# Kernel optimization log

Hardware: AMD Instinct MI355X
Metric: run time of the kernel (lower is better)

Reference implementation:

```python
import jax, jax.numpy as jnp
import numpy as np

N = 50000   # nodes
E = 800000  # edges (sparse adjacency nnz)
FI = 256    # input feature dim
FO = 64     # output feature dim per head
H = 8       # attention heads


def setup_inputs() -> dict:
    key = jax.random.key(0)
    ks = jax.random.split(key, 6)
    x = jax.random.normal(ks[0], (N, FI), dtype=jnp.float32)
    W = jax.random.normal(ks[1], (H, FI, FO), dtype=jnp.float32) * 0.05
    a = jax.random.normal(ks[2], (H, FO), dtype=jnp.float32) * 0.05
    b = jax.random.normal(ks[3], (H, FO), dtype=jnp.float32) * 0.05
    rows = jax.random.randint(ks[4], (E,), 0, N, dtype=jnp.int32)
    cols = jax.random.randint(ks[5], (E,), 0, N, dtype=jnp.int32)
    return {"x": x, "W": W, "a": a, "b": b, "rows": rows, "cols": cols}


def reference(x, W, a, b, rows, cols):
    # SparseGAT forward: per head linear -> edge scores -> sparse row softmax
    # -> sparse aggregation -> bias; heads averaged then ReLU.
    n = x.shape[0]
    h = W.shape[0]
    NEG_SLOPE = 0.2  # tf.nn.leaky_relu default alpha
    acc = None
    for i in range(h):  # small fixed loop over heads
        t = x @ W[i]                                   # [N, FO]
        aw = t @ a[i]                                  # [N]
        e = jax.nn.leaky_relu(aw[rows] + aw[cols], NEG_SLOPE)   # [E]
        # sparse softmax per row (segment softmax, numerically stable)
        m = jax.ops.segment_max(e, rows, num_segments=n)        # [N]
        ex = jnp.exp(e - m[rows])                                # [E]
        den = jax.ops.segment_sum(ex, rows, num_segments=n)      # [N]
        coef = ex / den[rows]                                    # [E]
        # sparse matmul: sum_j coef_ij * t_j
        agg = jax.ops.segment_sum(coef[:, None] * t[cols], rows, num_segments=n)
        agg = agg + b[i]
        acc = agg if acc is None else acc + agg
    return jax.nn.relu(acc / h)
```

## Files before the change

kernel.cpp:

```cpp
#include <hip/hip_runtime.h>
#include <hip/hip_bf16.h>
#include <hip/hip_fp16.h>


#define FI 256
#define FO 64
#define NH 8
#define FC 512
#define BM 128
#define NBIN 64

typedef _Float16 f16x8 __attribute__((ext_vector_type(8)));
typedef float f32x16 __attribute__((ext_vector_type(16)));
typedef float f32x8 __attribute__((ext_vector_type(8)));

__global__ __launch_bounds__(256)
void p1_wconv(const float* __restrict__ W, _Float16* __restrict__ Wth) {
  int idx = blockIdx.x * 256 + threadIdx.x;
  if (idx >= NH * FO * FI) return;
  int k = idx & (FI - 1);
  int f = (idx >> 8) & (FO - 1);
  int h = idx >> 14;
  Wth[idx] = (_Float16)W[((size_t)h * FI + k) * FO + f];
}

__global__ __launch_bounds__(512)
void k1_v3(const float* __restrict__ x, const _Float16* __restrict__ Wth,
           const float* __restrict__ a, _Float16* __restrict__ Th,
           float* __restrict__ aw, int N) {
  __shared__ _Float16 Xs[BM][136];
  const int bm = blockIdx.x * BM;
  const int t = threadIdx.x;
  const int w = t >> 6;
  const int lane = t & 63;
  const int l31 = lane & 31;
  const int hi = lane >> 5;
  const int kh = hi * 8;
  const _Float16* Wh = Wth + (size_t)w * (FO * FI);

  f32x16 acc[4][2];
  #pragma unroll
  for (int mr = 0; mr < 4; ++mr)
    #pragma unroll
    for (int wc = 0; wc < 2; ++wc) acc[mr][wc] = (f32x16)0.0f;

  #pragma unroll
  for (int k0 = 0; k0 < 2; ++k0) {
    if (k0) __syncthreads();
    #pragma unroll
    for (int r = 0; r < 8; ++r) {
      int i = t + r * 512;
      int row = i >> 5;
      int q = i & 31;
      float4 v = make_float4(0.f, 0.f, 0.f, 0.f);
      if (bm + row < N)
        v = reinterpret_cast<const float4*>(&x[(size_t)(bm + row) * FI + k0 * 128])[q];
      _Float16 o[4] = {(_Float16)v.x, (_Float16)v.y, (_Float16)v.z, (_Float16)v.w};
      *reinterpret_cast<uint2*>(&Xs[row][q * 4]) = *reinterpret_cast<uint2*>(o);
    }
    __syncthreads();
    #pragma unroll
    for (int kk = 0; kk < 8; ++kk) {
      f16x8 xf[4], wf[2];
      #pragma unroll
      for (int mr = 0; mr < 4; ++mr)
        xf[mr] = *reinterpret_cast<const f16x8*>(&Xs[mr * 32 + l31][kk * 16 + kh]);
      #pragma unroll
      for (int wc = 0; wc < 2; ++wc)
        wf[wc] = *reinterpret_cast<const f16x8*>(
            &Wh[(size_t)(wc * 32 + l31) * FI + k0 * 128 + kk * 16 + kh]);
      #pragma unroll
      for (int mr = 0; mr < 4; ++mr)
        #pragma unroll
        for (int wc = 0; wc < 2; ++wc)
          acc[mr][wc] =
              __builtin_amdgcn_mfma_f32_32x32x16_f16(wf[wc], xf[mr], acc[mr][wc], 0, 0, 0);
    }
  }


  float s4[4] = {0.f, 0.f, 0.f, 0.f};
  #pragma unroll
  for (int wc = 0; wc < 2; ++wc)
    #pragma unroll
    for (int reg = 0; reg < 16; ++reg) {
      float av = a[w * FO + wc * 32 + (reg & 3) + 8 * (reg >> 2) + 4 * hi];
      #pragma unroll
      for (int mr = 0; mr < 4; ++mr)
        s4[mr] = fmaf(acc[mr][wc][reg], av, s4[mr]);
    }
  #pragma unroll
  for (int mr = 0; mr < 4; ++mr) {
    float s = s4[mr] + __shfl_xor(s4[mr], 32);
    int n = bm + mr * 32 + l31;
    if (hi == 0 && n < N) aw[(size_t)n * NH + w] = s;
  }

  #pragma unroll
  for (int mr = 0; mr < 4; ++mr) {
    int n = bm + mr * 32 + l31;
    if (n >= N) continue;
    _Float16* rowp = Th + (size_t)n * FC + w * FO;
    #pragma unroll
    for (int wc = 0; wc < 2; ++wc)
      #pragma unroll
      for (int g = 0; g < 4; ++g) {
        _Float16 o[4] = {(_Float16)acc[mr][wc][4 * g + 0],
                         (_Float16)acc[mr][wc][4 * g + 1],
                         (_Float16)acc[mr][wc][4 * g + 2],
                         (_Float16)acc[mr][wc][4 * g + 3]};
        *reinterpret_cast<uint2*>(&rowp[wc * 32 + 8 * g + 4 * hi]) =
            *reinterpret_cast<uint2*>(o);
      }
  }
}

__global__ __launch_bounds__(256)
void b1_hist(const int* __restrict__ rows, int* __restrict__ deg, int E) {
  int e = blockIdx.x * 256 + threadIdx.x;
  if (e < E) atomicAdd(&deg[rows[e]], 1);
}

__global__ __launch_bounds__(256)
void b2a_blocksum(const int* __restrict__ deg, int* __restrict__ blocksums, int N) {
  __shared__ int red[256];
  const int t = threadIdx.x;
  const int base = blockIdx.x * 1024 + t * 4;
  int s = 0;
  #pragma unroll
  for (int j = 0; j < 4; ++j) { int i = base + j; if (i < N) s += deg[i]; }
  red[t] = s;
  __syncthreads();
  for (int off = 128; off; off >>= 1) {
    if (t < off) red[t] += red[t + off];
    __syncthreads();
  }
  if (t == 0) blocksums[blockIdx.x] = red[0];
}

__global__ __launch_bounds__(64)
void b2b_scanblocks(int* __restrict__ blocksums, int nb,
                    int* __restrict__ row_start, int N, int E) {
  const int lane = threadIdx.x;
  int carry = 0;
  for (int base = 0; base < nb; base += 64) {
    int i = base + lane;
    int v = (i < nb) ? blocksums[i] : 0;
    int inc = v;
    #pragma unroll
    for (int off = 1; off < 64; off <<= 1) {
      int t = __shfl_up(inc, off);
      if (lane >= off) inc += t;
    }
    if (i < nb) blocksums[i] = inc - v + carry;
    carry += __shfl(inc, 63);
  }
  if (lane == 0) row_start[N] = E;
}

__global__ __launch_bounds__(256)
void b2c_rescan(const int* __restrict__ deg, const int* __restrict__ blocksums,
                int* __restrict__ row_start, int* __restrict__ cursor,
                int* __restrict__ blockhist, int N, int nbp) {
  __shared__ int ts[256];
  __shared__ int hist[NBIN];
  const int t = threadIdx.x;
  const int base = blockIdx.x * 1024 + t * 4;
  if (t < NBIN) hist[t] = 0;
  int v[4]; int s = 0;
  #pragma unroll
  for (int j = 0; j < 4; ++j) { int i = base + j; v[j] = (i < N) ? deg[i] : 0; s += v[j]; }
  ts[t] = s;
  __syncthreads();
  for (int off = 1; off < 256; off <<= 1) {
    int add = (t >= off) ? ts[t - off] : 0;
    __syncthreads();
    ts[t] += add;
    __syncthreads();
  }
  int run = blocksums[blockIdx.x] + ts[t] - s;
  #pragma unroll
  for (int j = 0; j < 4; ++j) {
    int i = base + j;
    if (i < N) {
      row_start[i] = run; cursor[i] = run; run += v[j];
      atomicAdd(&hist[min(v[j], NBIN - 1)], 1);
    }
  }
  __syncthreads();
  if (t < NBIN) blockhist[t * nbp + blockIdx.x] = hist[t];
}

__global__ __launch_bounds__(256)
void b3_scatter(const int* __restrict__ rows, const int* __restrict__ cols,
                int* __restrict__ cursor, int* __restrict__ colperm, int E) {
  int e = blockIdx.x * 256 + threadIdx.x;
  if (e >= E) return;
  int pos = atomicAdd(&cursor[rows[e]], 1);
  colperm[pos] = cols[e];
}

__global__ __launch_bounds__(64)
void b5b_scan(int* __restrict__ blockhist, int nbp) {
  const int lane = threadIdx.x;
  int* rowp = blockhist + lane * nbp;
  int tot = 0;
  for (int c = 0; c < nbp / 4; ++c) {
    int4 v = reinterpret_cast<const int4*>(rowp)[c];
    tot += v.x + v.y + v.z + v.w;
  }
  int inc = tot;
  #pragma unroll
  for (int off = 1; off < 64; off <<= 1) {
    int t = __shfl_up(inc, off);
    if (lane >= off) inc += t;
  }
  int run = inc - tot;
  for (int c = 0; c < nbp / 4; ++c) {
    int4 v = reinterpret_cast<const int4*>(rowp)[c];
    int4 o;
    o.x = run; run += v.x;
    o.y = run; run += v.y;
    o.z = run; run += v.z;
    o.w = run; run += v.w;
    reinterpret_cast<int4*>(rowp)[c] = o;
  }
}

__global__ __launch_bounds__(256)
void b5c_scatter(const int* __restrict__ deg, const int* __restrict__ blockhist,
                 int* __restrict__ row_order, int N, int nbp) {
  __shared__ int cur[NBIN];
  const int t = threadIdx.x;
  if (t < NBIN) cur[t] = blockhist[t * nbp + blockIdx.x];
  __syncthreads();
  const int base = blockIdx.x * 1024 + t * 4;
  #pragma unroll
  for (int j = 0; j < 4; ++j) {
    int i = base + j;
    if (i < N) {
      int pos = atomicAdd(&cur[min(deg[i], NBIN - 1)], 1);
      row_order[pos] = i;
    }
  }
}

__global__ __launch_bounds__(256)
void k4_fused(const int* __restrict__ row_start, const int* __restrict__ colperm,
              const int* __restrict__ row_order,
              const float* __restrict__ aw, const _Float16* __restrict__ Th,
              const float* __restrict__ b, float* __restrict__ out, int N) {
  const int lane16 = threadIdx.x & 15;
  const int gbase  = threadIdx.x & 48;
  const int hi8    = lane16 >> 3;
  const int ri = blockIdx.x * 16 + (threadIdx.x >> 4);
  if (ri >= N) return;
  const int r = row_order[ri];

  const int s0 = row_start[r], s1 = row_start[r + 1];
  f32x8 awr = *reinterpret_cast<const f32x8*>(&aw[(size_t)r * NH]);

  float facc[4][8] = {};
  float dacc[NH] = {};

  for (int base = s0; base < s1; base += 16) {
    const int mm = min(16, s1 - base);
    const bool valid = lane16 < mm;
    int c_l = valid ? colperm[base + lane16] : 0;

    f32x8 awc = *reinterpret_cast<const f32x8*>(&aw[(size_t)c_l * NH]);
    float ex[NH];
    int pkv[4];
    #pragma unroll
    for (int h = 0; h < NH; ++h) {
      float s = awr[h] + awc[h];
      float lr = s > 0.f ? s : 0.2f * s;
      ex[h] = valid ? __expf(lr) : 0.f;
      dacc[h] += ex[h];
    }
    #pragma unroll
    for (int q = 0; q < 4; ++q) {
      __half2 h2 = __floats2half2_rn(ex[2 * q], ex[2 * q + 1]);
      pkv[q] = *reinterpret_cast<int*>(&h2);
    }

    for (int j = 0; j < mm; ++j) {
      int cj = __shfl(c_l, gbase + j);
      const _Float16* tp = Th + (size_t)cj * FC + lane16 * 8;
      f16x8 tv0 = *reinterpret_cast<const f16x8*>(tp);
      f16x8 tv1 = *reinterpret_cast<const f16x8*>(tp + 128);
      f16x8 tv2 = *reinterpret_cast<const f16x8*>(tp + 256);
      f16x8 tv3 = *reinterpret_cast<const f16x8*>(tp + 384);
      float eq[4];
      #pragma unroll
      for (int q = 0; q < 4; ++q) {
        int p = __shfl(pkv[q], gbase + j);
        float2 f2 = __half22float2(*reinterpret_cast<__half2*>(&p));
        eq[q] = hi8 ? f2.y : f2.x;
      }
      #pragma unroll
      for (int e = 0; e < 8; ++e) {
        facc[0][e] = fmaf(eq[0], (float)tv0[e], facc[0][e]);
        facc[1][e] = fmaf(eq[1], (float)tv1[e], facc[1][e]);
        facc[2][e] = fmaf(eq[2], (float)tv2[e], facc[2][e]);
        facc[3][e] = fmaf(eq[3], (float)tv3[e], facc[3][e]);
      }
    }
  }

  #pragma unroll
  for (int h = 0; h < NH; ++h) {
    #pragma unroll
    for (int off = 1; off < 16; off <<= 1)
      dacc[h] += __shfl_xor(dacc[h], off);
  }
  float rden[NH];
  #pragma unroll
  for (int h = 0; h < NH; ++h) rden[h] = dacc[h] > 0.f ? 1.0f / dacc[h] : 0.f;

  float s[8] = {};
  #pragma unroll
  for (int q = 0; q < 4; ++q) {
    float rd = hi8 ? rden[2 * q + 1] : rden[2 * q];
    #pragma unroll
    for (int e = 0; e < 8; ++e) s[e] = fmaf(facc[q][e], rd, s[e]);
  }
  #pragma unroll
  for (int e = 0; e < 8; ++e) s[e] += __shfl_xor(s[e], 8);

  if (lane16 < 8) {
    #pragma unroll
    for (int e = 0; e < 8; ++e) {
      const int f = lane16 * 8 + e;
      float sb = 0.f;
      #pragma unroll
      for (int h = 0; h < NH; ++h) sb += b[h * FO + f];
      float v = (s[e] + sb) * 0.125f;
      out[(size_t)r * FO + f] = v > 0.f ? v : 0.f;
    }
  }
}

extern "C" void kernel_launch(void* const* d_in, const int* in_sizes, int n_in,
                              void* d_out, int out_size, void* d_ws, size_t ws_size,
                              hipStream_t stream) {
  const float* x    = (const float*)d_in[0];
  const float* W    = (const float*)d_in[1];
  const float* a    = (const float*)d_in[2];
  const float* b    = (const float*)d_in[3];
  const int*   rows = (const int*)d_in[4];
  const int*   cols = (const int*)d_in[5];
  const int N = in_sizes[0] / FI;
  const int E = in_sizes[4];

  const int nb  = (N + 1023) / 1024;
  const int nbp = ((nb + 3) / 4) * 4;

  char* p = (char*)d_ws;
  _Float16* Th       = (_Float16*)p;  p += (size_t)N * FC * sizeof(_Float16);
  _Float16* Wth      = (_Float16*)p;  p += (size_t)NH * FO * FI * sizeof(_Float16);
  float*    aw       = (float*)p;     p += (size_t)N * NH * sizeof(float);
  int*      deg      = (int*)p;       p += (size_t)N * sizeof(int);
  int*      row_start= (int*)p;       p += (size_t)(N + 4) * sizeof(int);
  int*      cursor   = (int*)p;       p += (size_t)N * sizeof(int);
  int*      colperm  = (int*)p;       p += (size_t)E * sizeof(int);
  int*      blocksums= (int*)p;       p += 64 * sizeof(int);
  int*      row_order= (int*)p;       p += (size_t)N * sizeof(int);
  int*      blockhist= (int*)p;       p += (size_t)NBIN * nbp * sizeof(int);
  float*    out = (float*)d_out;

  hipMemsetAsync(deg, 0, (size_t)N * sizeof(int), stream);
  hipMemsetAsync(blockhist, 0, (size_t)NBIN * nbp * sizeof(int), stream);
  b1_hist<<<(E + 255) / 256, 256, 0, stream>>>(rows, deg, E);
  b2a_blocksum<<<nb, 256, 0, stream>>>(deg, blocksums, N);
  b2b_scanblocks<<<1, 64, 0, stream>>>(blocksums, nb, row_start, N, E);
  b2c_rescan<<<nb, 256, 0, stream>>>(deg, blocksums, row_start, cursor,
                                     blockhist, N, nbp);
  b3_scatter<<<(E + 255) / 256, 256, 0, stream>>>(rows, cols, cursor, colperm, E);
  b5b_scan<<<1, 64, 0, stream>>>(blockhist, nbp);
  b5c_scatter<<<nb, 256, 0, stream>>>(deg, blockhist, row_order, N, nbp);

  p1_wconv<<<(NH * FO * FI + 255) / 256, 256, 0, stream>>>(W, Wth);
  k1_v3<<<(N + BM - 1) / BM, 512, 0, stream>>>(x, Wth, a, Th, aw, N);

  k4_fused<<<(N + 15) / 16, 256, 0, stream>>>(row_start, colperm, row_order,
                                              aw, Th, b, out, N);
}
```

Baseline: 285.2 us.

## Fuse CSR-build kernels, merge memsets, and order rows by descending degree

Result: slower. 297.6 us (+4.3%).

```diff
diff --git a/kernel.cpp b/kernel.cpp
--- a/kernel.cpp
+++ b/kernel.cpp
@@ -78,7 +78,6 @@
     }
   }
 
-
   float s4[4] = {0.f, 0.f, 0.f, 0.f};
   #pragma unroll
   for (int wc = 0; wc < 2; ++wc)
@@ -122,47 +121,9 @@
 }
 
 __global__ __launch_bounds__(256)
-void b2a_blocksum(const int* __restrict__ deg, int* __restrict__ blocksums, int N) {
+void b2a_blocksum(const int* __restrict__ deg, int* __restrict__ blocksums,
+                  int* __restrict__ blockhist, int N, int nbp) {
   __shared__ int red[256];
-  const int t = threadIdx.x;
-  const int base = blockIdx.x * 1024 + t * 4;
-  int s = 0;
-  #pragma unroll
-  for (int j = 0; j < 4; ++j) { int i = base + j; if (i < N) s += deg[i]; }
-  red[t] = s;
-  __syncthreads();
-  for (int off = 128; off; off >>= 1) {
-    if (t < off) red[t] += red[t + off];
-    __syncthreads();
-  }
-  if (t == 0) blocksums[blockIdx.x] = red[0];
-}
-
-__global__ __launch_bounds__(64)
-void b2b_scanblocks(int* __restrict__ blocksums, int nb,
-                    int* __restrict__ row_start, int N, int E) {
-  const int lane = threadIdx.x;
-  int carry = 0;
-  for (int base = 0; base < nb; base += 64) {
-    int i = base + lane;
-    int v = (i < nb) ? blocksums[i] : 0;
-    int inc = v;
-    #pragma unroll
-    for (int off = 1; off < 64; off <<= 1) {
-      int t = __shfl_up(inc, off);
-      if (lane >= off) inc += t;
-    }
-    if (i < nb) blocksums[i] = inc - v + carry;
-    carry += __shfl(inc, 63);
-  }
-  if (lane == 0) row_start[N] = E;
-}
-
-__global__ __launch_bounds__(256)
-void b2c_rescan(const int* __restrict__ deg, const int* __restrict__ blocksums,
-                int* __restrict__ row_start, int* __restrict__ cursor,
-                int* __restrict__ blockhist, int N, int nbp) {
-  __shared__ int ts[256];
   __shared__ int hist[NBIN];
   const int t = threadIdx.x;
   const int base = blockIdx.x * 1024 + t * 4;
@@ -170,6 +131,76 @@
   int v[4]; int s = 0;
   #pragma unroll
   for (int j = 0; j < 4; ++j) { int i = base + j; v[j] = (i < N) ? deg[i] : 0; s += v[j]; }
+  __syncthreads();
+  #pragma unroll
+  for (int j = 0; j < 4; ++j)
+    if (base + j < N) atomicAdd(&hist[min(v[j], NBIN - 1)], 1);
+  red[t] = s;
+  __syncthreads();
+  for (int off = 128; off; off >>= 1) {
+    if (t < off) red[t] += red[t + off];
+    __syncthreads();
+  }
+  if (t == 0) blocksums[blockIdx.x] = red[0];
+  if (t < NBIN) blockhist[t * nbp + blockIdx.x] = hist[t];
+}
+
+__global__ __launch_bounds__(128)
+void b2b5b_scan(int* __restrict__ blocksums, int nb,
+                int* __restrict__ row_start, int N, int E,
+                int* __restrict__ blockhist, int nbp) {
+  const int w = threadIdx.x >> 6;
+  const int lane = threadIdx.x & 63;
+  if (w == 0) {
+    int carry = 0;
+    for (int base = 0; base < nb; base += 64) {
+      int i = base + lane;
+      int v = (i < nb) ? blocksums[i] : 0;
+      int inc = v;
+      #pragma unroll
+      for (int off = 1; off < 64; off <<= 1) {
+        int t = __shfl_up(inc, off);
+        if (lane >= off) inc += t;
+      }
+      if (i < nb) blocksums[i] = inc - v + carry;
+      carry += __shfl(inc, 63);
+    }
+    if (lane == 0) row_start[N] = E;
+  } else {
+    int* rowp = blockhist + (size_t)(NBIN - 1 - lane) * nbp;
+    int tot = 0;
+    for (int c = 0; c < nbp / 4; ++c) {
+      int4 v = reinterpret_cast<const int4*>(rowp)[c];
+      tot += v.x + v.y + v.z + v.w;
+    }
+    int inc = tot;
+    #pragma unroll
+    for (int off = 1; off < 64; off <<= 1) {
+      int t = __shfl_up(inc, off);
+      if (lane >= off) inc += t;
+    }
+    int run = inc - tot;
+    for (int c = 0; c < nbp / 4; ++c) {
+      int4 v = reinterpret_cast<const int4*>(rowp)[c];
+      int4 o;
+      o.x = run; run += v.x;
+      o.y = run; run += v.y;
+      o.z = run; run += v.z;
+      o.w = run; run += v.w;
+      reinterpret_cast<int4*>(rowp)[c] = o;
+    }
+  }
+}
+
+__global__ __launch_bounds__(256)
+void b2c_rescan(const int* __restrict__ deg, const int* __restrict__ blocksums,
+                int* __restrict__ row_start, int* __restrict__ cursor, int N) {
+  __shared__ int ts[256];
+  const int t = threadIdx.x;
+  const int base = blockIdx.x * 1024 + t * 4;
+  int v[4]; int s = 0;
+  #pragma unroll
+  for (int j = 0; j < 4; ++j) { int i = base + j; v[j] = (i < N) ? deg[i] : 0; s += v[j]; }
   ts[t] = s;
   __syncthreads();
   for (int off = 1; off < 256; off <<= 1) {
@@ -182,65 +213,34 @@
   #pragma unroll
   for (int j = 0; j < 4; ++j) {
     int i = base + j;
-    if (i < N) {
-      row_start[i] = run; cursor[i] = run; run += v[j];
-      atomicAdd(&hist[min(v[j], NBIN - 1)], 1);
-    }
-  }
-  __syncthreads();
-  if (t < NBIN) blockhist[t * nbp + blockIdx.x] = hist[t];
-}
-
-__global__ __launch_bounds__(256)
-void b3_scatter(const int* __restrict__ rows, const int* __restrict__ cols,
-                int* __restrict__ cursor, int* __restrict__ colperm, int E) {
-  int e = blockIdx.x * 256 + threadIdx.x;
-  if (e >= E) return;
-  int pos = atomicAdd(&cursor[rows[e]], 1);
-  colperm[pos] = cols[e];
-}
-
-__global__ __launch_bounds__(64)
-void b5b_scan(int* __restrict__ blockhist, int nbp) {
-  const int lane = threadIdx.x;
-  int* rowp = blockhist + lane * nbp;
-  int tot = 0;
-  for (int c = 0; c < nbp / 4; ++c) {
-    int4 v = reinterpret_cast<const int4*>(rowp)[c];
-    tot += v.x + v.y + v.z + v.w;
-  }
-  int inc = tot;
-  #pragma unroll
-  for (int off = 1; off < 64; off <<= 1) {
-    int t = __shfl_up(inc, off);
-    if (lane >= off) inc += t;
-  }
-  int run = inc - tot;
-  for (int c = 0; c < nbp / 4; ++c) {
-    int4 v = reinterpret_cast<const int4*>(rowp)[c];
-    int4 o;
-    o.x = run; run += v.x;
-    o.y = run; run += v.y;
-    o.z = run; run += v.z;
-    o.w = run; run += v.w;
-    reinterpret_cast<int4*>(rowp)[c] = o;
-  }
-}
-
-__global__ __launch_bounds__(256)
-void b5c_scatter(const int* __restrict__ deg, const int* __restrict__ blockhist,
-                 int* __restrict__ row_order, int N, int nbp) {
+    if (i < N) { row_start[i] = run; cursor[i] = run; run += v[j]; }
+  }
+}
+
+__global__ __launch_bounds__(256)
+void b3b5c_scatter(const int* __restrict__ rows, const int* __restrict__ cols,
+                   int* __restrict__ cursor, int* __restrict__ colperm, int E,
+                   const int* __restrict__ deg, const int* __restrict__ blockhist,
+                   int* __restrict__ row_order, int N, int nbp, int nb) {
   __shared__ int cur[NBIN];
   const int t = threadIdx.x;
-  if (t < NBIN) cur[t] = blockhist[t * nbp + blockIdx.x];
-  __syncthreads();
-  const int base = blockIdx.x * 1024 + t * 4;
-  #pragma unroll
-  for (int j = 0; j < 4; ++j) {
-    int i = base + j;
-    if (i < N) {
-      int pos = atomicAdd(&cur[min(deg[i], NBIN - 1)], 1);
-      row_order[pos] = i;
+  if ((int)blockIdx.x < nb) {
+    if (t < NBIN) cur[t] = blockhist[t * nbp + blockIdx.x];
+    __syncthreads();
+    const int base = blockIdx.x * 1024 + t * 4;
+    #pragma unroll
+    for (int j = 0; j < 4; ++j) {
+      int i = base + j;
+      if (i < N) {
+        int pos = atomicAdd(&cur[min(deg[i], NBIN - 1)], 1);
+        row_order[pos] = i;
+      }
+    }
+  } else {
+    int e = (blockIdx.x - nb) * 256 + t;
+    if (e < E) {
+      int pos = atomicAdd(&cursor[rows[e]], 1);
+      colperm[pos] = cols[e];
     }
   }
 }
@@ -361,24 +361,21 @@
   _Float16* Wth      = (_Float16*)p;  p += (size_t)NH * FO * FI * sizeof(_Float16);
   float*    aw       = (float*)p;     p += (size_t)N * NH * sizeof(float);
   int*      deg      = (int*)p;       p += (size_t)N * sizeof(int);
+  int*      blockhist= (int*)p;       p += (size_t)NBIN * nbp * sizeof(int);
   int*      row_start= (int*)p;       p += (size_t)(N + 4) * sizeof(int);
   int*      cursor   = (int*)p;       p += (size_t)N * sizeof(int);
   int*      colperm  = (int*)p;       p += (size_t)E * sizeof(int);
   int*      blocksums= (int*)p;       p += 64 * sizeof(int);
   int*      row_order= (int*)p;       p += (size_t)N * sizeof(int);
-  int*      blockhist= (int*)p;       p += (size_t)NBIN * nbp * sizeof(int);
   float*    out = (float*)d_out;
 
-  hipMemsetAsync(deg, 0, (size_t)N * sizeof(int), stream);
-  hipMemsetAsync(blockhist, 0, (size_t)NBIN * nbp * sizeof(int), stream);
+  hipMemsetAsync(deg, 0, ((size_t)N + (size_t)NBIN * nbp) * sizeof(int), stream);
   b1_hist<<<(E + 255) / 256, 256, 0, stream>>>(rows, deg, E);
-  b2a_blocksum<<<nb, 256, 0, stream>>>(deg, blocksums, N);
-  b2b_scanblocks<<<1, 64, 0, stream>>>(blocksums, nb, row_start, N, E);
-  b2c_rescan<<<nb, 256, 0, stream>>>(deg, blocksums, row_start, cursor,
-                                     blockhist, N, nbp);
-  b3_scatter<<<(E + 255) / 256, 256, 0, stream>>>(rows, cols, cursor, colperm, E);
-  b5b_scan<<<1, 64, 0, stream>>>(blockhist, nbp);
-  b5c_scatter<<<nb, 256, 0, stream>>>(deg, blockhist, row_order, N, nbp);
+  b2a_blocksum<<<nb, 256, 0, stream>>>(deg, blocksums, blockhist, N, nbp);
+  b2b5b_scan<<<1, 128, 0, stream>>>(blocksums, nb, row_start, N, E, blockhist, nbp);
+  b2c_rescan<<<nb, 256, 0, stream>>>(deg, blocksums, row_start, cursor, N);
+  b3b5c_scatter<<<nb + (E + 255) / 256, 256, 0, stream>>>(
+      rows, cols, cursor, colperm, E, deg, blockhist, row_order, N, nbp, nb);
 
   p1_wconv<<<(NH * FO * FI + 255) / 256, 256, 0, stream>>>(W, Wth);
   k1_v3<<<(N + BM - 1) / BM, 512, 0, stream>>>(x, Wth, a, Th, aw, N);
```
